# Performance work log

Measured on AMD Instinct MI355X. Metric: run time of the kernel, lower is better.

The kernel has to match this reference:

```python
import jax, jax.numpy as jnp
import numpy as np

D_MODEL = 256

def setup_inputs() -> dict:
    key = jax.random.key(0)
    k_x, k_wqkv, k_bqkv, k_wp, k_bp = jax.random.split(key, 5)
    B, T, d = 4, 4096, D_MODEL
    bound_qkv = 1.0 / np.sqrt(d)
    return {
        "x": jax.random.normal(k_x, (B, T, d), dtype=jnp.float32),
        "W_qkv": jax.random.uniform(k_wqkv, (d, 3 * d), jnp.float32, -bound_qkv, bound_qkv),
        "b_qkv": jax.random.uniform(k_bqkv, (3 * d,), jnp.float32, -bound_qkv, bound_qkv),
        "W_proj": jax.random.uniform(k_wp, (d, d), jnp.float32, -bound_qkv, bound_qkv),
        "b_proj": jax.random.uniform(k_bp, (d,), jnp.float32, -bound_qkv, bound_qkv),
    }

def reference(x, W_qkv, b_qkv, W_proj, b_proj):
    B, T, d = x.shape
    qkv = x @ W_qkv + b_qkv                       # (B, T, 3d)
    q, k, v = jnp.split(qkv, 3, axis=-1)          # each (B, T, d)
    scale = 1.0 / np.sqrt(d).astype(np.float32)
    scores = jnp.einsum('btd,bsd->bts', q, k) * scale   # (B, T, T)
    causal = jnp.tril(jnp.ones((T, T), dtype=bool))     # allowed positions
    scores = jnp.where(causal, scores, -jnp.inf)
    weights = jax.nn.softmax(scores, axis=-1)           # (B, T, T)
    ctx = jnp.einsum('bts,bsd->btd', weights, v)        # (B, T, d)
    return ctx @ W_proj + b_proj
```

## Files before the change

kernel.cpp:

```cpp
#include <hip/hip_runtime.h>
#include <math.h>

#define TT 4096
#define BB 4
#define DM 256
#define NSEG_B 144

typedef __attribute__((ext_vector_type(8))) short short8;
typedef __attribute__((ext_vector_type(4))) short short4v;
typedef __attribute__((ext_vector_type(4))) float f32x4;

#define MFMA16(a, b, c) __builtin_amdgcn_mfma_f32_16x16x32_bf16(a, b, c, 0, 0, 0)

#define GL2LDS(gp, lp) __builtin_amdgcn_global_load_lds( \
    (const __attribute__((address_space(1))) unsigned int*)(gp), \
    (__attribute__((address_space(3))) unsigned int*)(lp), 16, 0, 0)

__device__ __forceinline__ short f2b(float f) {
    union { float f; unsigned u; } v; v.f = f;
    unsigned r = v.u + 0x7FFFu + ((v.u >> 16) & 1u);
    return (short)(r >> 16);
}

__global__ __launch_bounds__(256) void transpose_cast2(
    const float* __restrict__ W1, short* __restrict__ Wt1,
    const float* __restrict__ W2, short* __restrict__ Wt2)
{
    __shared__ float T[64 * 68];
    const int tid = threadIdx.x;
    const int by = blockIdx.y;
    const float* W; short* Wt; int N, n0;
    if (by < 12) { W = W1; Wt = Wt1; N = 768; n0 = by * 64; }
    else         { W = W2; Wt = Wt2; N = 256; n0 = (by - 12) * 64; }
    const int k0 = blockIdx.x * 64;
#pragma unroll
    for (int it = 0; it < 4; ++it) {
        int idx = tid + it * 256;
        int r = idx >> 4, c4 = idx & 15;
        *(float4*)&T[r * 68 + c4 * 4] =
            *(const float4*)&W[(size_t)(k0 + r) * N + n0 + c4 * 4];
    }
    __syncthreads();
#pragma unroll
    for (int it = 0; it < 4; ++it) {
        int idx = tid + it * 256;
        int n = idx >> 4, c4 = idx & 15;
        short4v t;
#pragma unroll
        for (int j = 0; j < 4; ++j) t[j] = f2b(T[(c4 * 4 + j) * 68 + n]);
        *(short4v*)&Wt[(size_t)(n0 + n) * 256 + k0 + c4 * 4] = t;
    }
}

__global__ __launch_bounds__(256) void qkv_gemm(
    const float* __restrict__ x, const short* __restrict__ Bt,
    const float* __restrict__ bias, short* __restrict__ qkvb,
    short* __restrict__ VtG)
{
    __shared__ short As[16384];
    __shared__ short Bs[16384];
    __shared__ short Ts[64 * 72];

    const int tid = threadIdx.x;
    const int w = tid >> 6, lane = tid & 63;
    const int l15 = lane & 15, quad = lane >> 4;
    const int m0 = blockIdx.x * 64;
    const int nsup = blockIdx.y * 384;

#pragma unroll
    for (int it = 0; it < 8; ++it) {
        int idx = tid + it * 256;
        int row = ((idx >> 9) << 4) + (idx & 15);
        int col = ((idx >> 6) & 7) * 32 + ((idx >> 4) & 3) * 8;
        const float* src = &x[(size_t)(m0 + row) * 256 + col];
        float4 u = *(const float4*)src, u2 = *(const float4*)(src + 4);
        short8 t;
        t[0] = f2b(u.x);  t[1] = f2b(u.y);  t[2] = f2b(u.z);  t[3] = f2b(u.w);
        t[4] = f2b(u2.x); t[5] = f2b(u2.y); t[6] = f2b(u2.z); t[7] = f2b(u2.w);
        *(short8*)&As[idx * 8] = t;
    }

    for (int t6 = 0; t6 < 6; ++t6) {
        const int n0 = nsup + t6 * 64;
#pragma unroll
        for (int it = 0; it < 8; ++it) {
            int idx = tid + it * 256;
            int n = ((idx >> 9) << 4) + (idx & 15);
            int col = ((idx >> 6) & 7) * 32 + ((idx >> 4) & 3) * 8;
            *(short8*)&Bs[idx * 8] = *(const short8*)&Bt[(size_t)(n0 + n) * 256 + col];
        }
        __syncthreads();

        f32x4 acc[4];
#pragma unroll
        for (int t = 0; t < 4; ++t) acc[t] = (f32x4){0.f, 0.f, 0.f, 0.f};
#pragma unroll
        for (int k0 = 0; k0 < 8; ++k0) {
            short8 a = *(const short8*)&As[((w * 8 + k0) * 64 + lane) * 8];
#pragma unroll
            for (int nt = 0; nt < 4; ++nt) {
                short8 bb = *(const short8*)&Bs[((nt * 8 + k0) * 64 + lane) * 8];
                acc[nt] = MFMA16(a, bb, acc[nt]);
            }
        }

        if (n0 < 512) {
#pragma unroll
            for (int nt = 0; nt < 4; ++nt) {
                int n = n0 + nt * 16 + l15;
                float bv = bias[n];
#pragma unroll
                for (int r = 0; r < 4; ++r)
                    qkvb[(size_t)(m0 + w * 16 + quad * 4 + r) * 768 + n]
                        = f2b(acc[nt][r] + bv);
            }
            __syncthreads();
        } else {
#pragma unroll
            for (int nt = 0; nt < 4; ++nt) {
                int n = n0 + nt * 16 + l15;
                float bv = bias[n];
#pragma unroll
                for (int r = 0; r < 4; ++r)
                    Ts[(nt * 16 + l15) * 72 + w * 16 + quad * 4 + r]
                        = f2b(acc[nt][r] + bv);
            }
            __syncthreads();
            const int d  = tid >> 2;
            const int c  = tid & 3;
            short8 v0 = *(const short8*)&Ts[d * 72 + c * 16];
            short8 v1 = *(const short8*)&Ts[d * 72 + c * 16 + 8];
            const int bg = m0 >> 12, key0 = (m0 & 4095) + c * 16;
            short* dst = &VtG[((size_t)bg * 256 + (n0 - 512) + d) * 4096 + key0];
            *(short8*)dst = v0;
            *(short8*)(dst + 8) = v1;
        }
    }
}

__global__ __launch_bounds__(256, 2) void flash_mfma(
    const short* __restrict__ qkv,
    const short* __restrict__ VtG,
    float* __restrict__ Opart,
    float* __restrict__ L)
{
    __shared__ short Ks[2][4096];
    __shared__ short Vs[8192];
    __shared__ short Ps[4096];

    const int tid = threadIdx.x;
    const int w = tid >> 6, lane = tid & 63;
    const int l15 = lane & 15, quad = lane >> 4;

    const int b = blockIdx.x & 3;
    const int e = (NSEG_B - 1) - (blockIdx.x >> 2);
    const int lid = b * NSEG_B + e;
    int g = 0;
    while (g < 7 && e >= 2 * (g + 1) * (g + 2)) ++g;
    int off = e - 2 * g * (g + 1);
    int qt = 4 * g + off / (g + 1);
    int s  = off - (off / (g + 1)) * (g + 1);
    const int kp_lo = s * 16;
    const int kp_hi = min(kp_lo + 16, 4 * (qt + 1));
    const int npairs = kp_hi - kp_lo;

    const size_t base = (size_t)b * TT * 768;
    const int row0 = qt * 128;

    short8 aq[2][8];
#pragma unroll
    for (int rs = 0; rs < 2; ++rs) {
        const short* qrow = &qkv[base + (size_t)(row0 + rs * 64 + w * 16 + l15) * 768 + quad * 8];
#pragma unroll
        for (int k0 = 0; k0 < 8; ++k0)
            aq[rs][k0] = *(const short8*)&qrow[k0 * 32];
    }

#pragma unroll
    for (int it = 0; it < 2; ++it) {
        int idx = tid + it * 256;
        int row = idx & 15;
        int col = ((idx >> 6) & 7) * 32 + ((idx >> 4) & 3) * 8;
        GL2LDS(&qkv[base + (size_t)(kp_lo * 32 + row) * 768 + 256 + col], &Ks[0][idx * 8]);
    }

    f32x4 o[2][16];
#pragma unroll
    for (int rs = 0; rs < 2; ++rs)
#pragma unroll
        for (int c = 0; c < 16; ++c) o[rs][c] = (f32x4){0.f, 0.f, 0.f, 0.f};
    float l_acc[2][4] = {{0.f, 0.f, 0.f, 0.f}, {0.f, 0.f, 0.f, 0.f}};

    for (int u = 0; u < npairs; ++u) {
        const int j0 = (kp_lo + u) * 32;

        __syncthreads();

#pragma unroll
        for (int it = 0; it < 2; ++it) {
            int idx = tid + it * 256;
            int row = idx & 15;
            int col = ((idx >> 6) & 7) * 32 + ((idx >> 4) & 3) * 8;
            GL2LDS(&qkv[base + (size_t)(j0 + 16 + row) * 768 + 256 + col], &Ks[1][idx * 8]);
        }
        __builtin_amdgcn_sched_barrier(0);
#pragma unroll
        for (int it = 0; it < 4; ++it) {
            int idx = tid + it * 256;
            int d  = ((idx >> 6) << 4) + (idx & 15);
            int kc = ((idx >> 4) & 3) * 8;
            GL2LDS(&VtG[((size_t)b * 256 + d) * 4096 + j0 + kc], &Vs[idx * 8]);
        }
        __builtin_amdgcn_sched_barrier(0);

        {
            f32x4 s4[2];
            s4[0] = (f32x4){0.f, 0.f, 0.f, 0.f};
            s4[1] = (f32x4){0.f, 0.f, 0.f, 0.f};
#pragma unroll
            for (int k0 = 0; k0 < 8; ++k0) {
                short8 bb = *(const short8*)&Ks[0][(k0 * 64 + lane) * 8];
                s4[0] = MFMA16(aq[0][k0], bb, s4[0]);
                s4[1] = MFMA16(aq[1][k0], bb, s4[1]);
            }
#pragma unroll
            for (int rs = 0; rs < 2; ++rs)
#pragma unroll
                for (int r = 0; r < 4; ++r) {
                    const int rg = row0 + rs * 64 + w * 16 + quad * 4 + r;
                    int jg = j0 + l15;
                    float xx = s4[rs][r] * 0.0625f;
                    if (jg > rg) xx = -INFINITY;
                    float pv = __expf(fminf(xx, 30.f));
                    l_acc[rs][r] += pv;
                    Ps[((rs * 4 + w) * 64 + (0 * 2 + (l15 >> 3)) * 16 + quad * 4 + r) * 8
                       + (l15 & 7)] = f2b(pv);
                }
        }

        asm volatile("s_waitcnt vmcnt(4)" ::: "memory");
        __builtin_amdgcn_s_barrier();
        __builtin_amdgcn_sched_barrier(0);

        if (u + 1 < npairs) {
#pragma unroll
            for (int it = 0; it < 2; ++it) {
                int idx = tid + it * 256;
                int row = idx & 15;
                int col = ((idx >> 6) & 7) * 32 + ((idx >> 4) & 3) * 8;
                GL2LDS(&qkv[base + (size_t)(j0 + 32 + row) * 768 + 256 + col], &Ks[0][idx * 8]);
            }
        }
        __builtin_amdgcn_sched_barrier(0);

        {
            f32x4 s4[2];
            s4[0] = (f32x4){0.f, 0.f, 0.f, 0.f};
            s4[1] = (f32x4){0.f, 0.f, 0.f, 0.f};
#pragma unroll
            for (int k0 = 0; k0 < 8; ++k0) {
                short8 bb = *(const short8*)&Ks[1][(k0 * 64 + lane) * 8];
                s4[0] = MFMA16(aq[0][k0], bb, s4[0]);
                s4[1] = MFMA16(aq[1][k0], bb, s4[1]);
            }
#pragma unroll
            for (int rs = 0; rs < 2; ++rs)
#pragma unroll
                for (int r = 0; r < 4; ++r) {
                    const int rg = row0 + rs * 64 + w * 16 + quad * 4 + r;
                    int jg = j0 + 16 + l15;
                    float xx = s4[rs][r] * 0.0625f;
                    if (jg > rg) xx = -INFINITY;
                    float pv = __expf(fminf(xx, 30.f));
                    l_acc[rs][r] += pv;
                    Ps[((rs * 4 + w) * 64 + (1 * 2 + (l15 >> 3)) * 16 + quad * 4 + r) * 8
                       + (l15 & 7)] = f2b(pv);
                }
        }

        if (u + 1 < npairs) {
            asm volatile("s_waitcnt vmcnt(2)" ::: "memory");
        } else {
            asm volatile("s_waitcnt vmcnt(0)" ::: "memory");
        }
        __builtin_amdgcn_s_barrier();
        __builtin_amdgcn_sched_barrier(0);

        {
            short8 a0 = *(const short8*)&Ps[((0 * 4 + w) * 64 + lane) * 8];
            short8 a1 = *(const short8*)&Ps[((1 * 4 + w) * 64 + lane) * 8];
#pragma unroll
            for (int ct = 0; ct < 16; ++ct) {
                short8 bb = *(const short8*)&Vs[(ct * 64 + lane) * 8];
                o[0][ct] = MFMA16(a0, bb, o[0][ct]);
                o[1][ct] = MFMA16(a1, bb, o[1][ct]);
            }
        }
    }

#pragma unroll
    for (int rs = 0; rs < 2; ++rs)
#pragma unroll
        for (int r = 0; r < 4; ++r) {
            float l = l_acc[rs][r];
            l += __shfl_xor(l, 1); l += __shfl_xor(l, 2);
            l += __shfl_xor(l, 4); l += __shfl_xor(l, 8);
            if (l15 == 0)
                L[(size_t)lid * 128 + rs * 64 + w * 16 + quad * 4 + r] = l;
        }
    const size_t ob = (size_t)lid * (128 * 256);
#pragma unroll
    for (int rs = 0; rs < 2; ++rs)
#pragma unroll
        for (int r = 0; r < 4; ++r) {
            int lr = rs * 64 + w * 16 + quad * 4 + r;
#pragma unroll
            for (int c = 0; c < 16; ++c)
                Opart[ob + (size_t)lr * 256 + c * 16 + l15] = o[rs][c][r];
        }
}

__global__ __launch_bounds__(256) void proj_gemm(
    const float* __restrict__ Opart, const float* __restrict__ L,
    const short* __restrict__ Bt, const float* __restrict__ bias,
    float* __restrict__ out)
{
    __shared__ short As[8192];
    __shared__ short Bs[16384];
    __shared__ float Linv[32];

    const int tid = threadIdx.x;
    const int w = tid >> 6, lane = tid & 63;
    const int l15 = lane & 15, quad = lane >> 4;
    const int t = blockIdx.x;
    const int b = t >> 7, q32 = t & 127;
    const int qt = q32 >> 2;
    const int ro = (q32 & 3) * 32;
    const int gg = qt >> 2, rr = qt & 3;
    const int sbase = b * NSEG_B + 2 * gg * (gg + 1) + rr * (gg + 1);
    const int nseg = gg + 1;
    const int m0 = t * 32;

    if (tid < 32) {
        float l = 0.f;
#pragma unroll
        for (int s2 = 0; s2 < 8; ++s2)
            if (s2 < nseg) l += L[(size_t)(sbase + s2) * 128 + ro + tid];
        Linv[tid] = 1.f / l;
    }
    __syncthreads();

#pragma unroll
    for (int it = 0; it < 4; ++it) {
        int idx = tid + it * 256;
        int row = ((idx >> 9) << 4) + (idx & 15);
        int col = ((idx >> 6) & 7) * 32 + ((idx >> 4) & 3) * 8;
        float a8[8] = {0.f, 0.f, 0.f, 0.f, 0.f, 0.f, 0.f, 0.f};
#pragma unroll
        for (int s2 = 0; s2 < 8; ++s2) {
            if (s2 < nseg) {
                const float* src = &Opart[(size_t)(sbase + s2) * 32768
                                          + (size_t)(ro + row) * 256 + col];
                float4 u = *(const float4*)src, u2 = *(const float4*)(src + 4);
                a8[0] += u.x;  a8[1] += u.y;  a8[2] += u.z;  a8[3] += u.w;
                a8[4] += u2.x; a8[5] += u2.y; a8[6] += u2.z; a8[7] += u2.w;
            }
        }
        float inv = Linv[row];
        short8 t8;
#pragma unroll
        for (int j = 0; j < 8; ++j) t8[j] = f2b(a8[j] * inv);
        *(short8*)&As[idx * 8] = t8;
    }

    for (int t2 = 0; t2 < 4; ++t2) {
        const int n0 = t2 * 64;
#pragma unroll
        for (int it = 0; it < 8; ++it) {
            int idx = tid + it * 256;
            int n = ((idx >> 9) << 4) + (idx & 15);
            int col = ((idx >> 6) & 7) * 32 + ((idx >> 4) & 3) * 8;
            *(short8*)&Bs[idx * 8] = *(const short8*)&Bt[(size_t)(n0 + n) * 256 + col];
        }
        __syncthreads();

        f32x4 acc[2];
        acc[0] = (f32x4){0.f, 0.f, 0.f, 0.f};
        acc[1] = (f32x4){0.f, 0.f, 0.f, 0.f};
#pragma unroll
        for (int k0 = 0; k0 < 8; ++k0) {
            short8 a = *(const short8*)&As[(((w & 1) * 8 + k0) * 64 + lane) * 8];
#pragma unroll
            for (int nt = 0; nt < 2; ++nt) {
                int n16 = (w >> 1) * 2 + nt;
                short8 bb = *(const short8*)&Bs[((n16 * 8 + k0) * 64 + lane) * 8];
                acc[nt] = MFMA16(a, bb, acc[nt]);
            }
        }
#pragma unroll
        for (int nt = 0; nt < 2; ++nt) {
            int n = n0 + ((w >> 1) * 2 + nt) * 16 + l15;
            float bv = bias[n];
#pragma unroll
            for (int r = 0; r < 4; ++r)
                out[(size_t)(m0 + (w & 1) * 16 + quad * 4 + r) * 256 + n] = acc[nt][r] + bv;
        }
        __syncthreads();
    }
}

extern "C" void kernel_launch(void* const* d_in, const int* in_sizes, int n_in,
                              void* d_out, int out_size, void* d_ws, size_t ws_size,
                              hipStream_t stream)
{
    const float* x     = (const float*)d_in[0];
    const float* Wqkv  = (const float*)d_in[1];
    const float* bqkv  = (const float*)d_in[2];
    const float* Wproj = (const float*)d_in[3];
    const float* bproj = (const float*)d_in[4];
    float* out = (float*)d_out;

    const size_t M = (size_t)BB * TT;
    short* qkv_b = (short*)d_ws;
    short* Wt1   = qkv_b + M * 768;
    short* Wt2   = Wt1 + (size_t)768 * 256;
    short* VtG   = Wt2 + (size_t)256 * 256;
    float* Opart = (float*)(VtG + (size_t)BB * 256 * 4096);
    float* L     = Opart + (size_t)BB * NSEG_B * 128 * 256;

    transpose_cast2<<<dim3(4, 16), dim3(256), 0, stream>>>(Wqkv, Wt1, Wproj, Wt2);
    qkv_gemm<<<dim3(256, 2), dim3(256), 0, stream>>>(x, Wt1, bqkv, qkv_b, VtG);
    flash_mfma<<<dim3(BB * NSEG_B), dim3(256), 0, stream>>>(qkv_b, VtG, Opart, L);
    proj_gemm<<<dim3(512), dim3(256), 0, stream>>>(Opart, L, Wt2, bproj, out);
}
```

Baseline: 212.1 us.

## Deepen K/V prefetch pipeline with four-stage K ring and double-buffered V

Turns the K tile buffer into a four-slot ring and the V tile buffer into two slots. K and V for the next key pair are now issued one iteration ahead, and the prologue preloads the first pair. The s_waitcnt counts are changed to match the new number of loads in flight, and s_setprio is raised around the MFMA loops. The aim is to hide global-to-LDS latency behind the score and PV matrix math. In exchange, LDS per block grows from about 40 KB to 72 KB, which may limit blocks per CU. Loads past the end of the sequence are clamped, so the last iterations issue extra redundant loads.

```diff
diff --git a/kernel.cpp b/kernel.cpp
--- a/kernel.cpp
+++ b/kernel.cpp
@@ -144,8 +144,8 @@
     float* __restrict__ Opart,
     float* __restrict__ L)
 {
-    __shared__ short Ks[2][4096];
-    __shared__ short Vs[8192];
+    __shared__ short Ks[4][4096];
+    __shared__ short Vs[2][8192];
     __shared__ short Ps[4096];
 
     const int tid = threadIdx.x;
@@ -183,6 +183,23 @@
         int col = ((idx >> 6) & 7) * 32 + ((idx >> 4) & 3) * 8;
         GL2LDS(&qkv[base + (size_t)(kp_lo * 32 + row) * 768 + 256 + col], &Ks[0][idx * 8]);
     }
+    __builtin_amdgcn_sched_barrier(0);
+#pragma unroll
+    for (int it = 0; it < 2; ++it) {
+        int idx = tid + it * 256;
+        int row = idx & 15;
+        int col = ((idx >> 6) & 7) * 32 + ((idx >> 4) & 3) * 8;
+        GL2LDS(&qkv[base + (size_t)(kp_lo * 32 + 16 + row) * 768 + 256 + col], &Ks[1][idx * 8]);
+    }
+    __builtin_amdgcn_sched_barrier(0);
+#pragma unroll
+    for (int it = 0; it < 4; ++it) {
+        int idx = tid + it * 256;
+        int d  = ((idx >> 6) << 4) + (idx & 15);
+        int kc = ((idx >> 4) & 3) * 8;
+        GL2LDS(&VtG[((size_t)b * 256 + d) * 4096 + kp_lo * 32 + kc], &Vs[0][idx * 8]);
+    }
+    __builtin_amdgcn_sched_barrier(0);
 
     f32x4 o[2][16];
 #pragma unroll
@@ -193,36 +210,61 @@
 
     for (int u = 0; u < npairs; ++u) {
         const int j0 = (kp_lo + u) * 32;
-
-        __syncthreads();
-
-#pragma unroll
-        for (int it = 0; it < 2; ++it) {
-            int idx = tid + it * 256;
-            int row = idx & 15;
-            int col = ((idx >> 6) & 7) * 32 + ((idx >> 4) & 3) * 8;
-            GL2LDS(&qkv[base + (size_t)(j0 + 16 + row) * 768 + 256 + col], &Ks[1][idx * 8]);
-        }
+        const int pe  = (2 * u) & 3;
+        const int po  = (2 * u + 1) & 3;
+        const int pn2 = (2 * u + 2) & 3;
+        const int pn3 = (2 * u + 3) & 3;
+
+        {
+            int kb2 = min(j0 + 32, TT - 16);
+            int kb3 = min(j0 + 48, TT - 16);
+#pragma unroll
+            for (int it = 0; it < 2; ++it) {
+                int idx = tid + it * 256;
+                int row = idx & 15;
+                int col = ((idx >> 6) & 7) * 32 + ((idx >> 4) & 3) * 8;
+                GL2LDS(&qkv[base + (size_t)(kb2 + row) * 768 + 256 + col], &Ks[pn2][idx * 8]);
+            }
+            __builtin_amdgcn_sched_barrier(0);
+#pragma unroll
+            for (int it = 0; it < 2; ++it) {
+                int idx = tid + it * 256;
+                int row = idx & 15;
+                int col = ((idx >> 6) & 7) * 32 + ((idx >> 4) & 3) * 8;
+                GL2LDS(&qkv[base + (size_t)(kb3 + row) * 768 + 256 + col], &Ks[pn3][idx * 8]);
+            }
+            __builtin_amdgcn_sched_barrier(0);
+        }
+
+        asm volatile("s_waitcnt vmcnt(10)" ::: "memory");
+        __builtin_amdgcn_s_barrier();
         __builtin_amdgcn_sched_barrier(0);
-#pragma unroll
-        for (int it = 0; it < 4; ++it) {
-            int idx = tid + it * 256;
-            int d  = ((idx >> 6) << 4) + (idx & 15);
-            int kc = ((idx >> 4) & 3) * 8;
-            GL2LDS(&VtG[((size_t)b * 256 + d) * 4096 + j0 + kc], &Vs[idx * 8]);
-        }
-        __builtin_amdgcn_sched_barrier(0);
+
+        {
+            int vb = min(j0 + 32, TT - 32);
+#pragma unroll
+            for (int it = 0; it < 4; ++it) {
+                int idx = tid + it * 256;
+                int d  = ((idx >> 6) << 4) + (idx & 15);
+                int kc = ((idx >> 4) & 3) * 8;
+                GL2LDS(&VtG[((size_t)b * 256 + d) * 4096 + vb + kc],
+                       &Vs[(u + 1) & 1][idx * 8]);
+            }
+            __builtin_amdgcn_sched_barrier(0);
+        }
 
         {
             f32x4 s4[2];
             s4[0] = (f32x4){0.f, 0.f, 0.f, 0.f};
             s4[1] = (f32x4){0.f, 0.f, 0.f, 0.f};
+            __builtin_amdgcn_s_setprio(1);
 #pragma unroll
             for (int k0 = 0; k0 < 8; ++k0) {
-                short8 bb = *(const short8*)&Ks[0][(k0 * 64 + lane) * 8];
+                short8 bb = *(const short8*)&Ks[pe][(k0 * 64 + lane) * 8];
                 s4[0] = MFMA16(aq[0][k0], bb, s4[0]);
                 s4[1] = MFMA16(aq[1][k0], bb, s4[1]);
             }
+            __builtin_amdgcn_s_setprio(0);
 #pragma unroll
             for (int rs = 0; rs < 2; ++rs)
 #pragma unroll
@@ -238,31 +280,22 @@
                 }
         }
 
-        asm volatile("s_waitcnt vmcnt(4)" ::: "memory");
+        asm volatile("s_waitcnt vmcnt(12)" ::: "memory");
         __builtin_amdgcn_s_barrier();
-        __builtin_amdgcn_sched_barrier(0);
-
-        if (u + 1 < npairs) {
-#pragma unroll
-            for (int it = 0; it < 2; ++it) {
-                int idx = tid + it * 256;
-                int row = idx & 15;
-                int col = ((idx >> 6) & 7) * 32 + ((idx >> 4) & 3) * 8;
-                GL2LDS(&qkv[base + (size_t)(j0 + 32 + row) * 768 + 256 + col], &Ks[0][idx * 8]);
-            }
-        }
         __builtin_amdgcn_sched_barrier(0);
 
         {
             f32x4 s4[2];
             s4[0] = (f32x4){0.f, 0.f, 0.f, 0.f};
             s4[1] = (f32x4){0.f, 0.f, 0.f, 0.f};
+            __builtin_amdgcn_s_setprio(1);
 #pragma unroll
             for (int k0 = 0; k0 < 8; ++k0) {
-                short8 bb = *(const short8*)&Ks[1][(k0 * 64 + lane) * 8];
+                short8 bb = *(const short8*)&Ks[po][(k0 * 64 + lane) * 8];
                 s4[0] = MFMA16(aq[0][k0], bb, s4[0]);
                 s4[1] = MFMA16(aq[1][k0], bb, s4[1]);
             }
+            __builtin_amdgcn_s_setprio(0);
 #pragma unroll
             for (int rs = 0; rs < 2; ++rs)
 #pragma unroll
@@ -278,23 +311,21 @@
                 }
         }
 
-        if (u + 1 < npairs) {
-            asm volatile("s_waitcnt vmcnt(2)" ::: "memory");
-        } else {
-            asm volatile("s_waitcnt vmcnt(0)" ::: "memory");
-        }
+        asm volatile("s_waitcnt vmcnt(8)" ::: "memory");
         __builtin_amdgcn_s_barrier();
         __builtin_amdgcn_sched_barrier(0);
 
         {
             short8 a0 = *(const short8*)&Ps[((0 * 4 + w) * 64 + lane) * 8];
             short8 a1 = *(const short8*)&Ps[((1 * 4 + w) * 64 + lane) * 8];
+            __builtin_amdgcn_s_setprio(1);
 #pragma unroll
             for (int ct = 0; ct < 16; ++ct) {
-                short8 bb = *(const short8*)&Vs[(ct * 64 + lane) * 8];
+                short8 bb = *(const short8*)&Vs[u & 1][(ct * 64 + lane) * 8];
                 o[0][ct] = MFMA16(a0, bb, o[0][ct]);
                 o[1][ct] = MFMA16(a1, bb, o[1][ct]);
             }
+            __builtin_amdgcn_s_setprio(0);
         }
     }
 
```

After: 221.1 us. 4.2% more time.

## Process 64-key units per iteration with double-buffered K tiles

Applied to the files above, without the earlier changes.

Restructures the flash attention inner loop so each iteration handles 64 keys: four 16-row K sub-tiles and two V tiles. The next unit's K tiles are prefetched into a second buffer while the current unit computes. This halves the number of barriers per key and gives the loads more time to land before they are needed. In exchange, LDS use grows from about 40KB to about 112KB per block, which can lower the number of resident blocks per CU below the two requested in the launch bounds.

```diff
diff --git a/kernel.cpp b/kernel.cpp
--- a/kernel.cpp
+++ b/kernel.cpp
@@ -144,9 +144,9 @@
     float* __restrict__ Opart,
     float* __restrict__ L)
 {
-    __shared__ short Ks[2][4096];
-    __shared__ short Vs[8192];
-    __shared__ short Ps[4096];
+    __shared__ short Ks[2][4][4096];
+    __shared__ short Vs[2][8192];
+    __shared__ short Ps[2][4096];
 
     const int tid = threadIdx.x;
     const int w = tid >> 6, lane = tid & 63;
@@ -162,7 +162,7 @@
     int s  = off - (off / (g + 1)) * (g + 1);
     const int kp_lo = s * 16;
     const int kp_hi = min(kp_lo + 16, 4 * (qt + 1));
-    const int npairs = kp_hi - kp_lo;
+    const int nunits = (kp_hi - kp_lo) >> 1;
 
     const size_t base = (size_t)b * TT * 768;
     const int row0 = qt * 128;
@@ -177,121 +177,97 @@
     }
 
 #pragma unroll
-    for (int it = 0; it < 2; ++it) {
-        int idx = tid + it * 256;
-        int row = idx & 15;
-        int col = ((idx >> 6) & 7) * 32 + ((idx >> 4) & 3) * 8;
-        GL2LDS(&qkv[base + (size_t)(kp_lo * 32 + row) * 768 + 256 + col], &Ks[0][idx * 8]);
-    }
-
-    f32x4 o[2][16];
-#pragma unroll
-    for (int rs = 0; rs < 2; ++rs)
-#pragma unroll
-        for (int c = 0; c < 16; ++c) o[rs][c] = (f32x4){0.f, 0.f, 0.f, 0.f};
-    float l_acc[2][4] = {{0.f, 0.f, 0.f, 0.f}, {0.f, 0.f, 0.f, 0.f}};
-
-    for (int u = 0; u < npairs; ++u) {
-        const int j0 = (kp_lo + u) * 32;
-
-        __syncthreads();
-
+    for (int c = 0; c < 4; ++c) {
 #pragma unroll
         for (int it = 0; it < 2; ++it) {
             int idx = tid + it * 256;
             int row = idx & 15;
             int col = ((idx >> 6) & 7) * 32 + ((idx >> 4) & 3) * 8;
-            GL2LDS(&qkv[base + (size_t)(j0 + 16 + row) * 768 + 256 + col], &Ks[1][idx * 8]);
+            GL2LDS(&qkv[base + (size_t)(kp_lo * 32 + c * 16 + row) * 768 + 256 + col],
+                   &Ks[0][c][idx * 8]);
+        }
+    }
+    __builtin_amdgcn_sched_barrier(0);
+
+    f32x4 o[2][16];
+#pragma unroll
+    for (int rs = 0; rs < 2; ++rs)
+#pragma unroll
+        for (int c = 0; c < 16; ++c) o[rs][c] = (f32x4){0.f, 0.f, 0.f, 0.f};
+    float l_acc[2][4] = {{0.f, 0.f, 0.f, 0.f}, {0.f, 0.f, 0.f, 0.f}};
+
+    for (int u = 0; u < nunits; ++u) {
+        const int j0 = (kp_lo + 2 * u) * 32;
+        const int p = u & 1;
+
+        __syncthreads();
+
+#pragma unroll
+        for (int gv = 0; gv < 2; ++gv) {
+#pragma unroll
+            for (int it = 0; it < 4; ++it) {
+                int idx = tid + it * 256;
+                int d  = ((idx >> 6) << 4) + (idx & 15);
+                int kc = ((idx >> 4) & 3) * 8;
+                GL2LDS(&VtG[((size_t)b * 256 + d) * 4096 + j0 + gv * 32 + kc],
+                       &Vs[gv][idx * 8]);
+            }
         }
         __builtin_amdgcn_sched_barrier(0);
-#pragma unroll
-        for (int it = 0; it < 4; ++it) {
-            int idx = tid + it * 256;
-            int d  = ((idx >> 6) << 4) + (idx & 15);
-            int kc = ((idx >> 4) & 3) * 8;
-            GL2LDS(&VtG[((size_t)b * 256 + d) * 4096 + j0 + kc], &Vs[idx * 8]);
+        {
+            const int j0n = (u + 1 < nunits) ? (j0 + 64) : j0;
+#pragma unroll
+            for (int c = 0; c < 4; ++c) {
+#pragma unroll
+                for (int it = 0; it < 2; ++it) {
+                    int idx = tid + it * 256;
+                    int row = idx & 15;
+                    int col = ((idx >> 6) & 7) * 32 + ((idx >> 4) & 3) * 8;
+                    GL2LDS(&qkv[base + (size_t)(j0n + c * 16 + row) * 768 + 256 + col],
+                           &Ks[p ^ 1][c][idx * 8]);
+                }
+            }
         }
         __builtin_amdgcn_sched_barrier(0);
 
-        {
+#pragma unroll
+        for (int ph = 0; ph < 4; ++ph) {
             f32x4 s4[2];
             s4[0] = (f32x4){0.f, 0.f, 0.f, 0.f};
             s4[1] = (f32x4){0.f, 0.f, 0.f, 0.f};
 #pragma unroll
             for (int k0 = 0; k0 < 8; ++k0) {
-                short8 bb = *(const short8*)&Ks[0][(k0 * 64 + lane) * 8];
+                short8 bb = *(const short8*)&Ks[p][ph][(k0 * 64 + lane) * 8];
                 s4[0] = MFMA16(aq[0][k0], bb, s4[0]);
                 s4[1] = MFMA16(aq[1][k0], bb, s4[1]);
             }
+            const int gI = ph >> 1, ntI = ph & 1;
 #pragma unroll
             for (int rs = 0; rs < 2; ++rs)
 #pragma unroll
                 for (int r = 0; r < 4; ++r) {
                     const int rg = row0 + rs * 64 + w * 16 + quad * 4 + r;
-                    int jg = j0 + l15;
+                    int jg = j0 + ph * 16 + l15;
                     float xx = s4[rs][r] * 0.0625f;
                     if (jg > rg) xx = -INFINITY;
                     float pv = __expf(fminf(xx, 30.f));
                     l_acc[rs][r] += pv;
-                    Ps[((rs * 4 + w) * 64 + (0 * 2 + (l15 >> 3)) * 16 + quad * 4 + r) * 8
-                       + (l15 & 7)] = f2b(pv);
+                    Ps[gI][((rs * 4 + w) * 64 + (ntI * 2 + (l15 >> 3)) * 16 + quad * 4 + r) * 8
+                           + (l15 & 7)] = f2b(pv);
                 }
         }
 
-        asm volatile("s_waitcnt vmcnt(4)" ::: "memory");
+        asm volatile("s_waitcnt vmcnt(8)" ::: "memory");
         __builtin_amdgcn_s_barrier();
         __builtin_amdgcn_sched_barrier(0);
 
-        if (u + 1 < npairs) {
-#pragma unroll
-            for (int it = 0; it < 2; ++it) {
-                int idx = tid + it * 256;
-                int row = idx & 15;
-                int col = ((idx >> 6) & 7) * 32 + ((idx >> 4) & 3) * 8;
-                GL2LDS(&qkv[base + (size_t)(j0 + 32 + row) * 768 + 256 + col], &Ks[0][idx * 8]);
-            }
-        }
-        __builtin_amdgcn_sched_barrier(0);
-
-        {
-            f32x4 s4[2];
-            s4[0] = (f32x4){0.f, 0.f, 0.f, 0.f};
-            s4[1] = (f32x4){0.f, 0.f, 0.f, 0.f};
-#pragma unroll
-            for (int k0 = 0; k0 < 8; ++k0) {
-                short8 bb = *(const short8*)&Ks[1][(k0 * 64 + lane) * 8];
-                s4[0] = MFMA16(aq[0][k0], bb, s4[0]);
-                s4[1] = MFMA16(aq[1][k0], bb, s4[1]);
-            }
-#pragma unroll
-            for (int rs = 0; rs < 2; ++rs)
-#pragma unroll
-                for (int r = 0; r < 4; ++r) {
-                    const int rg = row0 + rs * 64 + w * 16 + quad * 4 + r;
-                    int jg = j0 + 16 + l15;
-                    float xx = s4[rs][r] * 0.0625f;
-                    if (jg > rg) xx = -INFINITY;
-                    float pv = __expf(fminf(xx, 30.f));
-                    l_acc[rs][r] += pv;
-                    Ps[((rs * 4 + w) * 64 + (1 * 2 + (l15 >> 3)) * 16 + quad * 4 + r) * 8
-                       + (l15 & 7)] = f2b(pv);
-                }
-        }
-
-        if (u + 1 < npairs) {
-            asm volatile("s_waitcnt vmcnt(2)" ::: "memory");
-        } else {
-            asm volatile("s_waitcnt vmcnt(0)" ::: "memory");
-        }
-        __builtin_amdgcn_s_barrier();
-        __builtin_amdgcn_sched_barrier(0);
-
-        {
-            short8 a0 = *(const short8*)&Ps[((0 * 4 + w) * 64 + lane) * 8];
-            short8 a1 = *(const short8*)&Ps[((1 * 4 + w) * 64 + lane) * 8];
+#pragma unroll
+        for (int gv = 0; gv < 2; ++gv) {
+            short8 a0 = *(const short8*)&Ps[gv][((0 * 4 + w) * 64 + lane) * 8];
+            short8 a1 = *(const short8*)&Ps[gv][((1 * 4 + w) * 64 + lane) * 8];
 #pragma unroll
             for (int ct = 0; ct < 16; ++ct) {
-                short8 bb = *(const short8*)&Vs[(ct * 64 + lane) * 8];
+                short8 bb = *(const short8*)&Vs[gv][(ct * 64 + lane) * 8];
                 o[0][ct] = MFMA16(a0, bb, o[0][ct]);
                 o[1][ct] = MFMA16(a1, bb, o[1][ct]);
             }
```

New measurement: 268.9 us. +26.8%, slower.
